# Performance work log

Hardware: AMD Instinct MI355X
Metric: run time of the kernel (lower is better)

The kernel has to match this reference:

```python
import jax, jax.numpy as jnp
import numpy as np

NUM_HEADS = 16  # matches init_kwargs num_heads


def setup_inputs() -> dict:
    key = jax.random.key(0)
    k0, k1, k2, k3, k4 = jax.random.split(key, 5)
    B, p, C = 8, 64, 1024
    N = p * p
    s = 1.0 / np.sqrt(C).astype(np.float32)
    return {
        "x": jax.random.normal(k0, (B, 3, N, C), jnp.float32),
        "wq": jax.random.normal(k1, (C, C), jnp.float32) * s,
        "wk": jax.random.normal(k2, (C, C), jnp.float32) * s,
        "wv": jax.random.normal(k3, (C, C), jnp.float32) * s,
        "w_proj": jax.random.normal(k4, (C, C), jnp.float32) * s,
        "b_proj": jnp.zeros((C,), jnp.float32),
    }


def reference(x, wq, wk, wv, w_proj, b_proj):
    # x: [B, 3, N, C] triplane tokens, N = p*p
    B, G, N, C = x.shape
    p = int(round(N ** 0.5))
    H = NUM_HEADS
    d = C // H
    scale = d ** -0.5

    xg = x.reshape(B, 3, p, p, C)
    # Linear projections are pointwise, so project each plane element once
    # (the torch code redundantly projects gathered copies; math is identical).
    qh = (xg @ wq.T).reshape(B, 3, p, p, H, d)
    kh = (xg @ wk.T).reshape(B, 3, p, p, H, d)
    vh = (xg @ wv.T).reshape(B, 3, p, p, H, d)

    outs = []
    for i in range(3):  # fixed loop over the 3 planes
        q_i = qh[:, i]                       # [B, a, j, H, d] query pixel (a, j)
        k_yz = kh[:, (i + 1) % 3]            # keys: row a of next plane -> [B, a, k, H, d]
        v_yz = vh[:, (i + 1) % 3]
        k_zx = kh[:, (i + 2) % 3]            # keys: column j of other plane -> [B, k, j, H, d]
        v_zx = vh[:, (i + 2) % 3]
        # scores against the p row-keys and p column-keys (2p keys total, 1 query)
        s1 = jnp.einsum('bajhd,bakhd->bajhk', q_i, k_yz) * scale
        s2 = jnp.einsum('bajhd,bkjhd->bajhk', q_i, k_zx) * scale
        attn = jax.nn.softmax(jnp.concatenate([s1, s2], axis=-1), axis=-1)  # [B,a,j,H,2p]
        a1, a2 = attn[..., :p], attn[..., p:]
        o = (jnp.einsum('bajhk,bakhd->bajhd', a1, v_yz)
             + jnp.einsum('bajhk,bkjhd->bajhd', a2, v_zx))  # [B,a,j,H,d]
        outs.append(o.reshape(B, N, C))
    # torch buffer is filled in [plane, B, N] order then reinterpreted as [B,3,N];
    # replicate that reshape quirk faithfully.
    out = jnp.stack(outs, axis=0)            # [3, B, N, C]
    out = out @ w_proj.T + b_proj
    return out.reshape(B, 3, N, C)
```

## Files before the change

### kernel.cpp

```cpp
#include <hip/hip_runtime.h>
#include <hip/hip_bf16.h>
#include <stdint.h>
#include <type_traits>

typedef __hip_bfloat16 hbf16;
typedef short bf16x8 __attribute__((ext_vector_type(8)));
typedef float f32x4 __attribute__((ext_vector_type(4)));
typedef unsigned int u32x4 __attribute__((ext_vector_type(4)));

#define MFMA16(a, b, c) __builtin_amdgcn_mfma_f32_16x16x32_bf16((a), (b), (c), 0, 0, 0)

__device__ __forceinline__ void gload_lds16(const void* g, void* l) {
  __builtin_amdgcn_global_load_lds(
      (const __attribute__((address_space(1))) void*)g,
      (__attribute__((address_space(3))) void*)l, 16, 0, 0);
}

__device__ __forceinline__ float b2f(unsigned short u) {
  union { unsigned int u32; float f; } cv;
  cv.u32 = ((unsigned int)u) << 16;
  return cv.f;
}
__device__ __forceinline__ unsigned short f2b(float f) {
  hbf16 h = __float2bfloat16(f);
  return __builtin_bit_cast(unsigned short, h);
}

__device__ __forceinline__ int swz(int row, int col) {
  return row * 64 + (col ^ ((row & 7) << 3));
}

__global__ __launch_bounds__(256) void cvt_f32_bf16(
    const float* __restrict__ src, unsigned short* __restrict__ dst, long long n)
{
  const long long i0 = ((long long)blockIdx.x * 256 + threadIdx.x) * 8;
  const long long stride = (long long)gridDim.x * 2048;
  for (long long i = i0; i < n; i += stride) {
    const float4 a = *(const float4*)(src + i);
    const float4 b = *(const float4*)(src + i + 4);
    bf16x8 o;
    o[0] = (short)f2b(a.x); o[1] = (short)f2b(a.y);
    o[2] = (short)f2b(a.z); o[3] = (short)f2b(a.w);
    o[4] = (short)f2b(b.x); o[5] = (short)f2b(b.y);
    o[6] = (short)f2b(b.z); o[7] = (short)f2b(b.w);
    *(bf16x8*)(dst + i) = o;
  }
}

template <typename OutT>
__global__ __launch_bounds__(512, 4) void gemm_bt(
    const unsigned short* __restrict__ A,
    const unsigned short* __restrict__ W,
    const float* __restrict__ bias,
    OutT* __restrict__ C,
    int M, int N, int K)
{
  __shared__ __attribute__((aligned(16))) unsigned short Sm[36864];

  const int tid  = threadIdx.x;
  const int lane = tid & 63;
  const int w    = tid >> 6;
  const int wr64 = (w >> 1) * 64;
  const int wc64 = (w & 1) * 64;
  const int lr   = lane & 15;
  const int lg   = lane >> 4;
  const int wofs = w * 512;

  const int nwg     = gridDim.x;
  const int bx      = blockIdx.x;
  const int logical = (bx & 7) * (nwg >> 3) + (bx >> 3);
  const int colsN   = N >> 7;
  const int tileM   = logical / colsN;
  const int tileN   = logical - tileM * colsN;
  const size_t rowBase = (size_t)tileM * 256;
  const int    colBase = tileN * 128;

  const int sRow   = tid >> 2;
  const int sChunk = (tid & 3) ^ ((tid >> 3) & 3);
  const unsigned short* Ag0 = A + (rowBase + sRow) * (size_t)K + sChunk * 8;
  const unsigned short* Ag1 = Ag0 + (size_t)128 * K;
  const unsigned short* Wg0 = W + ((size_t)colBase + sRow) * K + sChunk * 8;

  f32x4 acc[4][4] = {};
  const int nt = K >> 5;

#pragma unroll
  for (int p = 0; p < 2; ++p) {
    const size_t ke = (size_t)p * 32;
    gload_lds16(Ag0 + ke, Sm + p * 8192 + wofs);
    gload_lds16(Ag1 + ke, Sm + p * 8192 + 4096 + wofs);
    gload_lds16(Wg0 + ke, Sm + 24576 + p * 4096 + wofs);
  }

#define GITER(T, VM, STG)                                                     \
  do {                                                                        \
    asm volatile("s_waitcnt vmcnt(" VM ")" ::: "memory");                     \
    __builtin_amdgcn_s_barrier();                                             \
    __builtin_amdgcn_sched_barrier(0);                                        \
    if (STG) {                                                                \
      const int nb = ((T) + 2) % 3;                                           \
      const size_t ke = (size_t)((T) + 2) * 32;                               \
      gload_lds16(Ag0 + ke, Sm + nb * 8192 + wofs);                           \
      gload_lds16(Ag1 + ke, Sm + nb * 8192 + 4096 + wofs);                    \
      gload_lds16(Wg0 + ke, Sm + 24576 + nb * 4096 + wofs);                   \
    }                                                                         \
    const unsigned short* asb = Sm + ((T) % 3) * 8192;                        \
    const unsigned short* bsb = Sm + 24576 + ((T) % 3) * 4096;                \
    bf16x8 af[4], bfv[4];                                                     \
    _Pragma("unroll")                                                         \
    for (int mi = 0; mi < 4; ++mi) {                                          \
      const int row = wr64 + mi * 16 + lr;                                    \
      af[mi] = *(const bf16x8*)(asb + row * 32 + (lg ^ ((row >> 1) & 3)) * 8);\
    }                                                                         \
    _Pragma("unroll")                                                         \
    for (int ni = 0; ni < 4; ++ni) {                                          \
      const int row = wc64 + ni * 16 + lr;                                    \
      bfv[ni] = *(const bf16x8*)(bsb + row * 32 + (lg ^ ((row >> 1) & 3)) * 8);\
    }                                                                         \
    _Pragma("unroll")                                                         \
    for (int mi = 0; mi < 4; ++mi)                                            \
      _Pragma("unroll")                                                       \
      for (int ni = 0; ni < 4; ++ni)                                          \
        acc[mi][ni] = MFMA16(af[mi], bfv[ni], acc[mi][ni]);                   \
  } while (0)

  for (int t = 0; t < nt - 2; ++t) GITER(t, "3", true);
  GITER(nt - 2, "3", false);
  GITER(nt - 1, "0", false);
#undef GITER

  __syncthreads();

  float bv[4];
#pragma unroll
  for (int ni = 0; ni < 4; ++ni)
    bv[ni] = bias ? bias[colBase + wc64 + ni * 16 + lr] : 0.0f;

  const size_t R0 = rowBase + wr64;
  const int    C0 = colBase + wc64;

#pragma unroll
  for (int batch = 0; batch < 2; ++batch) {
    if constexpr (std::is_same_v<OutT, float>) {
      float* reg = (float*)(void*)Sm + w * 2048;
#pragma unroll
      for (int mi2 = 0; mi2 < 2; ++mi2) {
        const int mi = batch * 2 + mi2;
#pragma unroll
        for (int ni = 0; ni < 4; ++ni)
#pragma unroll
          for (int r = 0; r < 4; ++r)
            reg[(mi2 * 16 + lg * 4 + r) * 64 + ni * 16 + lr] =
                acc[mi][ni][r] + bv[ni];
      }
      asm volatile("s_waitcnt lgkmcnt(0)" ::: "memory");
      __builtin_amdgcn_sched_barrier(0);
#pragma unroll
      for (int it = 0; it < 8; ++it) {
        const int ch  = it * 64 + lane;
        const int row = ch >> 4, cc = ch & 15;
        const float4 v = *(const float4*)(reg + row * 64 + cc * 4);
        *(float4*)((float*)C + (R0 + batch * 32 + row) * (size_t)N + C0 + cc * 4) = v;
      }
    } else {
      unsigned short* reg = Sm + w * 2048;
#pragma unroll
      for (int mi2 = 0; mi2 < 2; ++mi2) {
        const int mi = batch * 2 + mi2;
#pragma unroll
        for (int ni = 0; ni < 4; ++ni)
#pragma unroll
          for (int r = 0; r < 4; ++r)
            reg[(mi2 * 16 + lg * 4 + r) * 64 + ni * 16 + lr] =
                f2b(acc[mi][ni][r] + bv[ni]);
      }
      asm volatile("s_waitcnt lgkmcnt(0)" ::: "memory");
      __builtin_amdgcn_sched_barrier(0);
#pragma unroll
      for (int it = 0; it < 4; ++it) {
        const int ch  = it * 64 + lane;
        const int row = ch >> 3, cc = ch & 7;
        const u32x4 v = *(const u32x4*)(reg + row * 64 + cc * 8);
        *(u32x4*)((unsigned short*)C + (R0 + batch * 32 + row) * (size_t)N + C0 + cc * 8) = v;
      }
    }
  }
}

__global__ __launch_bounds__(256) void attn_yz(
    const unsigned short* __restrict__ Q,
    const unsigned short* __restrict__ Kx,
    const unsigned short* __restrict__ Vx,
    unsigned short* __restrict__ O1,
    float* __restrict__ m1s, float* __restrict__ l1s)
{
  __shared__ __attribute__((aligned(16))) unsigned short Qs[4096], Ks[4096], Vs[4096], Ps[4096];

  const int bid = blockIdx.x;
  const int h = bid & 15;
  const int a = (bid >> 4) & 63;
  const int b = (bid >> 10) & 7;
  const int i = bid >> 13;
  const int i1 = (i + 1) % 3;

  const size_t qoff = ((size_t)((b * 3 + i) * 4096 + a * 64)) * 1024 + h * 64;
  const size_t koff = ((size_t)((b * 3 + i1) * 4096 + a * 64)) * 1024 + h * 64;

  const int tid = threadIdx.x;
#pragma unroll
  for (int it = 0; it < 2; ++it) {
    const int idx = it * 2048 + tid * 8;
    const int row = idx >> 6, col = idx & 63;
    const int d = swz(row, col);
    *(bf16x8*)&Qs[d] = *(const bf16x8*)(Q + qoff + (size_t)row * 1024 + col);
    *(bf16x8*)&Ks[d] = *(const bf16x8*)(Kx + koff + (size_t)row * 1024 + col);
    *(bf16x8*)&Vs[d] = *(const bf16x8*)(Vx + koff + (size_t)row * 1024 + col);
  }
  __syncthreads();

  const int lane = tid & 63;
  const int w  = tid >> 6;
  const int lr = lane & 15;
  const int lg = lane >> 4;

  f32x4 sa[4] = {};
  {
    const bf16x8 aq0 = *(const bf16x8*)&Qs[swz(w * 16 + lr, lg * 8)];
    const bf16x8 aq1 = *(const bf16x8*)&Qs[swz(w * 16 + lr, 32 + lg * 8)];
#pragma unroll
    for (int nf = 0; nf < 4; ++nf) {
      const bf16x8 bk0 = *(const bf16x8*)&Ks[swz(nf * 16 + lr, lg * 8)];
      const bf16x8 bk1 = *(const bf16x8*)&Ks[swz(nf * 16 + lr, 32 + lg * 8)];
      sa[nf] = MFMA16(aq0, bk0, sa[nf]);
      sa[nf] = MFMA16(aq1, bk1, sa[nf]);
    }
  }

  const float scale = 0.125f;
  float m[4], ls[4];
#pragma unroll
  for (int r = 0; r < 4; ++r) {
#pragma unroll
    for (int nf = 0; nf < 4; ++nf) sa[nf][r] *= scale;
    float v = fmaxf(fmaxf(sa[0][r], sa[1][r]), fmaxf(sa[2][r], sa[3][r]));
    v = fmaxf(v, __shfl_xor(v, 1));
    v = fmaxf(v, __shfl_xor(v, 2));
    v = fmaxf(v, __shfl_xor(v, 4));
    v = fmaxf(v, __shfl_xor(v, 8));
    m[r] = v;
    float s = 0.0f;
#pragma unroll
    for (int nf = 0; nf < 4; ++nf) { const float p = __expf(sa[nf][r] - v); sa[nf][r] = p; s += p; }
    s += __shfl_xor(s, 1);
    s += __shfl_xor(s, 2);
    s += __shfl_xor(s, 4);
    s += __shfl_xor(s, 8);
    ls[r] = s;
  }

#pragma unroll
  for (int nf = 0; nf < 4; ++nf)
#pragma unroll
    for (int r = 0; r < 4; ++r)
      Ps[swz(w * 16 + lg * 4 + r, nf * 16 + lr)] = f2b(sa[nf][r]);

  if (lr == 0) {
    const size_t sb = ((size_t)(i * 8 + b) * 16 + h) * 4096 + a * 64 + w * 16 + lg * 4;
#pragma unroll
    for (int r = 0; r < 4; ++r) { m1s[sb + r] = m[r]; l1s[sb + r] = ls[r]; }
  }
  __syncthreads();

  f32x4 oa[4] = {};
#pragma unroll
  for (int ks = 0; ks < 2; ++ks) {
    const bf16x8 ap = *(const bf16x8*)&Ps[swz(w * 16 + lr, ks * 32 + lg * 8)];
#pragma unroll
    for (int df = 0; df < 4; ++df) {
      bf16x8 bv;
#pragma unroll
      for (int e = 0; e < 8; ++e)
        bv[e] = (short)Vs[swz(ks * 32 + lg * 8 + e, df * 16 + lr)];
      oa[df] = MFMA16(ap, bv, oa[df]);
    }
  }

  const size_t ob = ((size_t)(i * 8 + b) * 4096 + a * 64) * 1024 + h * 64;
#pragma unroll
  for (int df = 0; df < 4; ++df)
#pragma unroll
    for (int r = 0; r < 4; ++r)
      O1[ob + (size_t)(w * 16 + lg * 4 + r) * 1024 + df * 16 + lr] = f2b(oa[df][r]);
}

__global__ __launch_bounds__(256) void attn_zx(
    const unsigned short* __restrict__ Q,
    const unsigned short* __restrict__ Kx,
    const unsigned short* __restrict__ Vx,
    unsigned short* __restrict__ O1,
    const float* __restrict__ m1s, const float* __restrict__ l1s)
{
  __shared__ __attribute__((aligned(16))) unsigned short Qs[4096], Ks[4096], Vs[4096], Ps[4096];

  const int bid = blockIdx.x;
  const int j = bid & 63;
  const int h = (bid >> 6) & 15;
  const int b = (bid >> 10) & 7;
  const int i = bid >> 13;
  const int i2 = (i + 2) % 3;

  const size_t qoff = ((size_t)(b * 3 + i) * 4096 + j) * 1024 + h * 64;
  const size_t koff = ((size_t)(b * 3 + i2) * 4096 + j) * 1024 + h * 64;
  const size_t rstride = 65536;

  const int tid = threadIdx.x;
#pragma unroll
  for (int it = 0; it < 2; ++it) {
    const int idx = it * 2048 + tid * 8;
    const int row = idx >> 6, col = idx & 63;
    const int d = swz(row, col);
    *(bf16x8*)&Qs[d] = *(const bf16x8*)(Q + qoff + (size_t)row * rstride + col);
    *(bf16x8*)&Ks[d] = *(const bf16x8*)(Kx + koff + (size_t)row * rstride + col);
    *(bf16x8*)&Vs[d] = *(const bf16x8*)(Vx + koff + (size_t)row * rstride + col);
  }
  __syncthreads();

  const int lane = tid & 63;
  const int w  = tid >> 6;
  const int lr = lane & 15;
  const int lg = lane >> 4;

  f32x4 sa[4] = {};
  {
    const bf16x8 aq0 = *(const bf16x8*)&Qs[swz(w * 16 + lr, lg * 8)];
    const bf16x8 aq1 = *(const bf16x8*)&Qs[swz(w * 16 + lr, 32 + lg * 8)];
#pragma unroll
    for (int nf = 0; nf < 4; ++nf) {
      const bf16x8 bk0 = *(const bf16x8*)&Ks[swz(nf * 16 + lr, lg * 8)];
      const bf16x8 bk1 = *(const bf16x8*)&Ks[swz(nf * 16 + lr, 32 + lg * 8)];
      sa[nf] = MFMA16(aq0, bk0, sa[nf]);
      sa[nf] = MFMA16(aq1, bk1, sa[nf]);
    }
  }

  const float scale = 0.125f;
  float m[4], ls[4];
#pragma unroll
  for (int r = 0; r < 4; ++r) {
#pragma unroll
    for (int nf = 0; nf < 4; ++nf) sa[nf][r] *= scale;
    float v = fmaxf(fmaxf(sa[0][r], sa[1][r]), fmaxf(sa[2][r], sa[3][r]));
    v = fmaxf(v, __shfl_xor(v, 1));
    v = fmaxf(v, __shfl_xor(v, 2));
    v = fmaxf(v, __shfl_xor(v, 4));
    v = fmaxf(v, __shfl_xor(v, 8));
    m[r] = v;
    float s = 0.0f;
#pragma unroll
    for (int nf = 0; nf < 4; ++nf) { const float p = __expf(sa[nf][r] - v); sa[nf][r] = p; s += p; }
    s += __shfl_xor(s, 1);
    s += __shfl_xor(s, 2);
    s += __shfl_xor(s, 4);
    s += __shfl_xor(s, 8);
    ls[r] = s;
  }

  float c1[4], c2[4], rden[4];
  const size_t sb = ((size_t)(i * 8 + b) * 16 + h) * 4096 + j;
#pragma unroll
  for (int r = 0; r < 4; ++r) {
    const int arow = w * 16 + lg * 4 + r;
    const float mm1 = m1s[sb + (size_t)arow * 64];
    const float ll1 = l1s[sb + (size_t)arow * 64];
    const float mm = fmaxf(mm1, m[r]);
    const float e1 = __expf(mm1 - mm);
    const float e2 = __expf(m[r] - mm);
    c1[r] = e1; c2[r] = e2;
    rden[r] = 1.0f / (e1 * ll1 + e2 * ls[r]);
  }

#pragma unroll
  for (int nf = 0; nf < 4; ++nf)
#pragma unroll
    for (int r = 0; r < 4; ++r)
      Ps[swz(w * 16 + lg * 4 + r, nf * 16 + lr)] = f2b(sa[nf][r]);
  __syncthreads();

  f32x4 oa[4] = {};
#pragma unroll
  for (int ks = 0; ks < 2; ++ks) {
    const bf16x8 ap = *(const bf16x8*)&Ps[swz(w * 16 + lr, ks * 32 + lg * 8)];
#pragma unroll
    for (int df = 0; df < 4; ++df) {
      bf16x8 bv;
#pragma unroll
      for (int e = 0; e < 8; ++e)
        bv[e] = (short)Vs[swz(ks * 32 + lg * 8 + e, df * 16 + lr)];
      oa[df] = MFMA16(ap, bv, oa[df]);
    }
  }

  const size_t ob = ((size_t)(i * 8 + b) * 4096 + j) * 1024 + h * 64;
#pragma unroll
  for (int df = 0; df < 4; ++df)
#pragma unroll
    for (int r = 0; r < 4; ++r) {
      const size_t addr = ob + (size_t)(w * 16 + lg * 4 + r) * rstride + df * 16 + lr;
      const float o1v = b2f(O1[addr]);
      O1[addr] = f2b((c1[r] * o1v + c2[r] * oa[df][r]) * rden[r]);
    }
}

extern "C" void kernel_launch(void* const* d_in, const int* in_sizes, int n_in,
                              void* d_out, int out_size, void* d_ws, size_t ws_size,
                              hipStream_t stream)
{
  const float* x  = (const float*)d_in[0];
  const float* wq = (const float*)d_in[1];
  const float* wk = (const float*)d_in[2];
  const float* wv = (const float*)d_in[3];
  const float* wp = (const float*)d_in[4];
  const float* bp = (const float*)d_in[5];

  const int M = 98304, N = 1024, K = 1024;
  const size_t SLAB = 201326592ull;
  const size_t STAT = 6291456ull;

  char* ws = (char*)d_ws;
  unsigned short* xb  = (unsigned short*)(ws);
  unsigned short* Kb  = (unsigned short*)(ws + SLAB);
  unsigned short* Vb  = (unsigned short*)(ws + 2 * SLAB);
  float* m1s          = (float*)(ws + 3 * SLAB);
  float* l1s          = (float*)(ws + 3 * SLAB + STAT);
  unsigned short* wqb = (unsigned short*)(ws + 3 * SLAB + 2 * STAT);
  unsigned short* wkb = wqb + 1048576;
  unsigned short* wvb = wkb + 1048576;
  unsigned short* wpb = wvb + 1048576;
  unsigned short* Qb  = (unsigned short*)d_out;
  unsigned short* O1  = xb;

  dim3 blk(256);
  cvt_f32_bf16<<<dim3(4096), blk, 0, stream>>>(x,  xb,  (long long)M * 1024);
  cvt_f32_bf16<<<dim3(512),  blk, 0, stream>>>(wq, wqb, 1048576);
  cvt_f32_bf16<<<dim3(512),  blk, 0, stream>>>(wk, wkb, 1048576);
  cvt_f32_bf16<<<dim3(512),  blk, 0, stream>>>(wv, wvb, 1048576);
  cvt_f32_bf16<<<dim3(512),  blk, 0, stream>>>(wp, wpb, 1048576);

  dim3 gg((M / 256) * (N / 128));
  dim3 gblk(512);
  gemm_bt<unsigned short><<<gg, gblk, 0, stream>>>(xb, wqb, (const float*)nullptr, Qb, M, N, K);
  gemm_bt<unsigned short><<<gg, gblk, 0, stream>>>(xb, wkb, (const float*)nullptr, Kb, M, N, K);
  gemm_bt<unsigned short><<<gg, gblk, 0, stream>>>(xb, wvb, (const float*)nullptr, Vb, M, N, K);
  attn_yz<<<dim3(24576), blk, 0, stream>>>(Qb, Kb, Vb, O1, m1s, l1s);
  attn_zx<<<dim3(24576), blk, 0, stream>>>(Qb, Kb, Vb, O1, m1s, l1s);
  gemm_bt<float><<<gg, gblk, 0, stream>>>(O1, wpb, bp, (float*)d_out, M, N, K);
}
```

Measured before the change: 1.445 ms.

## Fuse Q/K/V projections into one GEMM over concatenated weights and batch weight conversion

After: 1.411 ms. 1.02x faster.

```diff
diff --git a/kernel.cpp b/kernel.cpp
--- a/kernel.cpp
+++ b/kernel.cpp
@@ -44,6 +44,144 @@
     o[4] = (short)f2b(b.x); o[5] = (short)f2b(b.y);
     o[6] = (short)f2b(b.z); o[7] = (short)f2b(b.w);
     *(bf16x8*)(dst + i) = o;
+  }
+}
+
+__global__ __launch_bounds__(256) void cvt4_w(
+    const float* __restrict__ s0, const float* __restrict__ s1,
+    const float* __restrict__ s2, const float* __restrict__ s3,
+    unsigned short* __restrict__ dst)
+{
+  const int q = blockIdx.x >> 9;
+  const float* src = (q == 0) ? s0 : (q == 1) ? s1 : (q == 2) ? s2 : s3;
+  const long long i = ((long long)(blockIdx.x & 511) * 256 + threadIdx.x) * 8;
+  const float4 a = *(const float4*)(src + i);
+  const float4 b = *(const float4*)(src + i + 4);
+  bf16x8 o;
+  o[0] = (short)f2b(a.x); o[1] = (short)f2b(a.y);
+  o[2] = (short)f2b(a.z); o[3] = (short)f2b(a.w);
+  o[4] = (short)f2b(b.x); o[5] = (short)f2b(b.y);
+  o[6] = (short)f2b(b.z); o[7] = (short)f2b(b.w);
+  *(bf16x8*)(dst + (long long)q * 1048576 + i) = o;
+}
+
+__global__ __launch_bounds__(256, 2) void gemm_qkv(
+    const unsigned short* __restrict__ A,
+    const unsigned short* __restrict__ W,
+    unsigned short* __restrict__ Cq,
+    unsigned short* __restrict__ Ck,
+    unsigned short* __restrict__ Cv,
+    int M, int Ntot, int K)
+{
+  __shared__ __attribute__((aligned(16))) unsigned short Sm[36864];
+
+  const int tid  = threadIdx.x;
+  const int lane = tid & 63;
+  const int w    = tid >> 6;
+  const int wr   = w >> 1;
+  const int wc   = w & 1;
+  const int lr   = lane & 15;
+  const int lg   = lane >> 4;
+
+  const int nwg     = gridDim.x;
+  const int bx      = blockIdx.x;
+  const int logical = (bx & 7) * (nwg >> 3) + (bx >> 3);
+  const int colsN   = Ntot >> 7;
+  const int tileM   = logical / colsN;
+  const int tileN   = logical - tileM * colsN;
+  const size_t rowBase = (size_t)tileM * 256;
+  const int    colBase = tileN * 128;
+
+  const int sRow   = tid >> 2;
+  const int sChunk = (tid & 3) ^ ((tid >> 3) & 3);
+  const unsigned short* Ag0 = A + (rowBase +   0 + sRow) * (size_t)K + sChunk * 8;
+  const unsigned short* Ag1 = A + (rowBase +  64 + sRow) * (size_t)K + sChunk * 8;
+  const unsigned short* Ag2 = A + (rowBase + 128 + sRow) * (size_t)K + sChunk * 8;
+  const unsigned short* Ag3 = A + (rowBase + 192 + sRow) * (size_t)K + sChunk * 8;
+  const unsigned short* Wg0 = W + ((size_t)colBase +  0 + sRow) * K + sChunk * 8;
+  const unsigned short* Wg1 = W + ((size_t)colBase + 64 + sRow) * K + sChunk * 8;
+
+  f32x4 acc[8][4] = {};
+  const int nt = K >> 5;
+
+#pragma unroll
+  for (int p = 0; p < 2; ++p) {
+    const size_t ke = (size_t)p * 32;
+    unsigned short* ab = Sm + p * 8192;
+    unsigned short* bb = Sm + 24576 + p * 4096;
+    gload_lds16(Ag0 + ke, ab +        w * 512);
+    gload_lds16(Ag1 + ke, ab + 2048 + w * 512);
+    gload_lds16(Ag2 + ke, ab + 4096 + w * 512);
+    gload_lds16(Ag3 + ke, ab + 6144 + w * 512);
+    gload_lds16(Wg0 + ke, bb +        w * 512);
+    gload_lds16(Wg1 + ke, bb + 2048 + w * 512);
+  }
+
+#define QITER(T, VM, STG)                                                     \
+  do {                                                                        \
+    asm volatile("s_waitcnt vmcnt(" VM ")" ::: "memory");                     \
+    __builtin_amdgcn_s_barrier();                                             \
+    __builtin_amdgcn_sched_barrier(0);                                        \
+    if (STG) {                                                                \
+      const int nb = ((T) + 2) % 3;                                           \
+      const size_t ke = (size_t)((T) + 2) * 32;                               \
+      unsigned short* ab = Sm + nb * 8192;                                    \
+      unsigned short* bb = Sm + 24576 + nb * 4096;                            \
+      gload_lds16(Ag0 + ke, ab +        w * 512);                             \
+      gload_lds16(Ag1 + ke, ab + 2048 + w * 512);                             \
+      gload_lds16(Ag2 + ke, ab + 4096 + w * 512);                             \
+      gload_lds16(Ag3 + ke, ab + 6144 + w * 512);                             \
+      gload_lds16(Wg0 + ke, bb +        w * 512);                             \
+      gload_lds16(Wg1 + ke, bb + 2048 + w * 512);                             \
+    }                                                                         \
+    const unsigned short* asb = Sm + ((T) % 3) * 8192;                        \
+    const unsigned short* bsb = Sm + 24576 + ((T) % 3) * 4096;                \
+    bf16x8 af[8], bfv[4];                                                     \
+    _Pragma("unroll")                                                         \
+    for (int mi = 0; mi < 8; ++mi) {                                          \
+      const int row = wr * 128 + mi * 16 + lr;                                \
+      af[mi] = *(const bf16x8*)(asb + row * 32 + (lg ^ ((row >> 1) & 3)) * 8);\
+    }                                                                         \
+    _Pragma("unroll")                                                         \
+    for (int ni = 0; ni < 4; ++ni) {                                          \
+      const int row = wc * 64 + ni * 16 + lr;                                 \
+      bfv[ni] = *(const bf16x8*)(bsb + row * 32 + (lg ^ ((row >> 1) & 3)) * 8);\
+    }                                                                         \
+    _Pragma("unroll")                                                         \
+    for (int mi = 0; mi < 8; ++mi)                                            \
+      _Pragma("unroll")                                                       \
+      for (int ni = 0; ni < 4; ++ni)                                          \
+        acc[mi][ni] = MFMA16(af[mi], bfv[ni], acc[mi][ni]);                   \
+  } while (0)
+
+  for (int t = 0; t < nt - 2; ++t) QITER(t, "6", true);
+  QITER(nt - 2, "6", false);
+  QITER(nt - 1, "0", false);
+#undef QITER
+
+  __syncthreads();
+  unsigned short* G = Sm + wr * 16384;
+#pragma unroll
+  for (int mi = 0; mi < 8; ++mi)
+#pragma unroll
+    for (int ni = 0; ni < 4; ++ni)
+#pragma unroll
+      for (int r = 0; r < 4; ++r) {
+        const int row = mi * 16 + lg * 4 + r;
+        const int c   = wc * 64 + ni * 16 + lr;
+        G[row * 128 + (c ^ (((row >> 2) & 3) << 4))] = f2b(acc[mi][ni][r]);
+      }
+  __syncthreads();
+
+  const int out = colBase >> 10;
+  unsigned short* Co = (out == 0) ? Cq : (out == 1) ? Ck : Cv;
+  const int colLocal = colBase & 1023;
+#pragma unroll
+  for (int it = 0; it < 16; ++it) {
+    const int ch  = it * 128 + wc * 64 + lane;
+    const int row = ch >> 4, cc = ch & 15;
+    const u32x4 v = *(const u32x4*)(G + row * 128 + ((cc * 8) ^ (((row >> 2) & 3) << 4)));
+    *(u32x4*)(Co + (rowBase + wr * 128 + row) * 1024 + colLocal + cc * 8) = v;
   }
 }
 
@@ -149,9 +287,11 @@
 #pragma unroll
         for (int ni = 0; ni < 4; ++ni)
 #pragma unroll
-          for (int r = 0; r < 4; ++r)
-            reg[(mi2 * 16 + lg * 4 + r) * 64 + ni * 16 + lr] =
+          for (int r = 0; r < 4; ++r) {
+            const int row = mi2 * 16 + lg * 4 + r;
+            reg[row * 64 + ((ni * 16 + lr) ^ (((row >> 2) & 3) << 4))] =
                 acc[mi][ni][r] + bv[ni];
+          }
       }
       asm volatile("s_waitcnt lgkmcnt(0)" ::: "memory");
       __builtin_amdgcn_sched_barrier(0);
@@ -159,7 +299,7 @@
       for (int it = 0; it < 8; ++it) {
         const int ch  = it * 64 + lane;
         const int row = ch >> 4, cc = ch & 15;
-        const float4 v = *(const float4*)(reg + row * 64 + cc * 4);
+        const float4 v = *(const float4*)(reg + row * 64 + ((cc * 4) ^ (((row >> 2) & 3) << 4)));
         *(float4*)((float*)C + (R0 + batch * 32 + row) * (size_t)N + C0 + cc * 4) = v;
       }
     } else {
@@ -433,25 +573,20 @@
   float* m1s          = (float*)(ws + 3 * SLAB);
   float* l1s          = (float*)(ws + 3 * SLAB + STAT);
   unsigned short* wqb = (unsigned short*)(ws + 3 * SLAB + 2 * STAT);
-  unsigned short* wkb = wqb + 1048576;
-  unsigned short* wvb = wkb + 1048576;
-  unsigned short* wpb = wvb + 1048576;
+  unsigned short* wpb = wqb + 3145728;
   unsigned short* Qb  = (unsigned short*)d_out;
   unsigned short* O1  = xb;
 
   dim3 blk(256);
-  cvt_f32_bf16<<<dim3(4096), blk, 0, stream>>>(x,  xb,  (long long)M * 1024);
-  cvt_f32_bf16<<<dim3(512),  blk, 0, stream>>>(wq, wqb, 1048576);
-  cvt_f32_bf16<<<dim3(512),  blk, 0, stream>>>(wk, wkb, 1048576);
-  cvt_f32_bf16<<<dim3(512),  blk, 0, stream>>>(wv, wvb, 1048576);
-  cvt_f32_bf16<<<dim3(512),  blk, 0, stream>>>(wp, wpb, 1048576);
-
-  dim3 gg((M / 256) * (N / 128));
-  dim3 gblk(512);
-  gemm_bt<unsigned short><<<gg, gblk, 0, stream>>>(xb, wqb, (const float*)nullptr, Qb, M, N, K);
-  gemm_bt<unsigned short><<<gg, gblk, 0, stream>>>(xb, wkb, (const float*)nullptr, Kb, M, N, K);
-  gemm_bt<unsigned short><<<gg, gblk, 0, stream>>>(xb, wvb, (const float*)nullptr, Vb, M, N, K);
+  cvt_f32_bf16<<<dim3(4096), blk, 0, stream>>>(x, xb, (long long)M * 1024);
+  cvt4_w<<<dim3(2048), blk, 0, stream>>>(wq, wk, wv, wp, wqb);
+
+  gemm_qkv<<<dim3((M / 256) * (3072 / 128)), dim3(256), 0, stream>>>(
+      xb, wqb, Qb, Kb, Vb, M, 3072, K);
+
   attn_yz<<<dim3(24576), blk, 0, stream>>>(Qb, Kb, Vb, O1, m1s, l1s);
   attn_zx<<<dim3(24576), blk, 0, stream>>>(Qb, Kb, Vb, O1, m1s, l1s);
-  gemm_bt<float><<<gg, gblk, 0, stream>>>(O1, wpb, bp, (float*)d_out, M, N, K);
-}
+
+  gemm_bt<float><<<dim3((M / 256) * (N / 128)), dim3(512), 0, stream>>>(
+      O1, wpb, bp, (float*)d_out, M, N, K);
+}
```
